# Kernel optimization log

Measured on AMD Instinct MI355X. Metric: run time of the kernel, lower is better.

## Reference

```python
import jax, jax.numpy as jnp
import numpy as np

# ---- static genetic-code tables (stand-in for CODON2ID / ID2AA / SYN_CODON) ----
N_CODONS = 65   # index 0 = pad
N_AA = 24       # ids 0..2 special, 3..22 = 20 amino acids, 23 = stop
_SIZES = np.array([4, 6, 2, 2, 2, 2, 2, 3, 2, 6, 1, 2, 4, 2, 6, 4, 4, 1, 2, 4, 3], dtype=np.int64)  # degeneracy per group (last = stop), sums to 64
_CODON2AA_np = np.concatenate([[0], np.repeat(np.arange(3, 24), _SIZES)])          # [65]
_NSYN_np = np.zeros(N_AA, dtype=np.float32)
_NSYN_np[3:23] = _SIZES[:20]                    # stop (23) and specials (<=2) -> 0, i.e. not in SYN_CODON
CODON2AA = jnp.asarray(_CODON2AA_np)            # [65] int
NSYN_CODON = jnp.asarray(_NSYN_np[_CODON2AA_np])  # [65] f32, n_synonymous for each codon's AA
_starts = 1 + np.concatenate([[0], np.cumsum(_SIZES)[:-1]])
_OFF_AA = np.zeros(N_AA, dtype=np.int64); _OFF_AA[3:24] = _starts
_SZ_AA = np.ones(N_AA, dtype=np.int64);  _SZ_AA[3:24] = _SIZES
OFF_AA = jnp.asarray(_OFF_AA)
SZ_AA = jnp.asarray(_SZ_AA)


def _sequence_rscu(codon_ids, mask):
    """Vectorized compute_sequence_rscu: histogram + per-AA grouped normalization."""
    B = codon_ids.shape[0]
    valid = mask & (codon_ids > 0)
    w = valid.astype(jnp.float32)
    # per-batch codon histogram: scatter-add of 1s over codon ids  [B, 65]
    counts = jnp.zeros((B, N_CODONS), jnp.float32).at[jnp.arange(B)[:, None], codon_ids].add(w)
    # per-AA total count via segment-reduce over the static codon->AA map  [B, 24]
    aa_tot = jnp.zeros((B, N_AA), jnp.float32).at[:, CODON2AA].add(counts)
    tot_c = aa_tot[:, CODON2AA]  # gather AA total back to codon axis  [B, 65]
    # rscu = count * n_synonymous / total_count_of_that_AA (0 where no observations / non-SYN AA)
    rscu = jnp.where(tot_c > 0, counts * NSYN_CODON / jnp.maximum(tot_c, 1.0), 0.0)
    return rscu


def setup_inputs() -> dict:
    key = jax.random.key(0)
    k1, k2, k3, k4, k5 = jax.random.split(key, 5)
    B, L, S = 512, 8192, 5
    target_codon_ids = jax.random.randint(k1, (B, L), 1, N_CODONS)
    aa_ids = CODON2AA[target_codon_ids]                       # consistent AA labels (>=3)
    r = jax.random.randint(k2, (B, L), 0, 6)
    pred_codon_ids = OFF_AA[aa_ids] + r % SZ_AA[aa_ids]       # synonymous predictions (same AA)
    mask = jax.random.uniform(k3, (B, L)) < 0.9
    species_ids = jax.random.randint(k4, (B,), 0, S)
    ref_distributions = jax.random.uniform(k5, (S, N_CODONS), minval=0.0, maxval=2.0)
    return dict(pred_codon_ids=pred_codon_ids, target_codon_ids=target_codon_ids,
                aa_ids=aa_ids, species_ids=species_ids, mask=mask,
                ref_distributions=ref_distributions)


def reference(pred_codon_ids, target_codon_ids, aa_ids, species_ids, mask, ref_distributions):
    pred_rscu = _sequence_rscu(pred_codon_ids, mask)
    target_rscu = _sequence_rscu(target_codon_ids, mask)
    n_species = ref_distributions.shape[0]
    in_range = (species_ids >= 0) & (species_ids < n_species)
    ref_rscu = jnp.where(in_range[:, None],
                         ref_distributions[jnp.clip(species_ids, 0, n_species - 1)], 0.0)
    combined_target = 0.7 * target_rscu + 0.3 * ref_rscu
    p = pred_rscu + 1e-8
    t = combined_target + 1e-8
    p = p / p.sum(axis=1, keepdims=True)
    t = t / t.sum(axis=1, keepdims=True)
    kl_div = (t * jnp.log(t / p)).sum(axis=1)  # [B]
    return kl_div
```

## Files before the change

kernel.cpp:

```cpp
#include <hip/hip_runtime.h>

#define N_CODONS 65
#define N_AA 24

__constant__ int c_codon2aa[N_CODONS] = {
    0,
    3,3,3,3,
    4,4,4,4,4,4,
    5,5,
    6,6,
    7,7,
    8,8,
    9,9,
    10,10,10,
    11,11,
    12,12,12,12,12,12,
    13,
    14,14,
    15,15,15,15,
    16,16,
    17,17,17,17,17,17,
    18,18,18,18,
    19,19,19,19,
    20,
    21,21,
    22,22,22,22,
    23,23,23
};

__constant__ float c_nsyn[N_CODONS] = {
    0.f,
    4.f,4.f,4.f,4.f,
    6.f,6.f,6.f,6.f,6.f,6.f,
    2.f,2.f,
    2.f,2.f,
    2.f,2.f,
    2.f,2.f,
    2.f,2.f,
    3.f,3.f,3.f,
    2.f,2.f,
    6.f,6.f,6.f,6.f,6.f,6.f,
    1.f,
    2.f,2.f,
    4.f,4.f,4.f,4.f,
    2.f,2.f,
    6.f,6.f,6.f,6.f,6.f,6.f,
    4.f,4.f,4.f,4.f,
    4.f,4.f,4.f,4.f,
    1.f,
    2.f,2.f,
    4.f,4.f,4.f,4.f,
    0.f,0.f,0.f
};

__device__ __forceinline__ float wave_sum64(float v) {
#pragma unroll
    for (int off = 32; off > 0; off >>= 1)
        v += __shfl_xor(v, off, 64);
    return v;
}

__global__ __launch_bounds__(1024)
void rscu_kl_kernel(const int* __restrict__ pred,
                    const int* __restrict__ targ,
                    const int* __restrict__ mask,
                    const int* __restrict__ species,
                    const float* __restrict__ ref,
                    float* __restrict__ out,
                    int L, int n_species)
{
    const int b    = blockIdx.x;
    const int tid  = threadIdx.x;
    const int lane = tid & 63;

    __shared__ unsigned int h[2][16][N_CODONS];
    __shared__ float pr[N_CODONS];
    __shared__ float tr[N_CODONS];
    __shared__ float aaP[N_AA], aaT[N_AA];

    for (int i = tid; i < 2 * 16 * N_CODONS; i += 1024)
        ((unsigned int*)h)[i] = 0u;
    if (tid < N_AA) { aaP[tid] = 0.f; aaT[tid] = 0.f; }
    __syncthreads();

    const int4* p4 = (const int4*)(pred + (size_t)b * L);
    const int4* t4 = (const int4*)(targ + (size_t)b * L);
    const int4* m4 = (const int4*)(mask + (size_t)b * L);
    const int nvec = L >> 2;

    unsigned int* hp = &h[0][lane >> 2][0];
    unsigned int* ht = &h[1][lane >> 2][0];
    const unsigned int inc = 1u << ((lane & 3) * 8);

    for (int i = tid; i < nvec; i += 1024) {
        int4 pv = p4[i];
        int4 tv = t4[i];
        int4 mv = m4[i];
        int bp0 = mv.x ? pv.x : 0;  int bt0 = mv.x ? tv.x : 0;
        int bp1 = mv.y ? pv.y : 0;  int bt1 = mv.y ? tv.y : 0;
        int bp2 = mv.z ? pv.z : 0;  int bt2 = mv.z ? tv.z : 0;
        int bp3 = mv.w ? pv.w : 0;  int bt3 = mv.w ? tv.w : 0;
        atomicAdd(hp + bp0, inc);   atomicAdd(ht + bt0, inc);
        atomicAdd(hp + bp1, inc);   atomicAdd(ht + bt1, inc);
        atomicAdd(hp + bp2, inc);   atomicAdd(ht + bt2, inc);
        atomicAdd(hp + bp3, inc);   atomicAdd(ht + bt3, inc);
    }
    __syncthreads();

    if (tid < N_CODONS) {
        unsigned int sp = 0u, st = 0u;
#pragma unroll
        for (int g = 0; g < 16; ++g) {
            unsigned int wp = h[0][g][tid];
            unsigned int wt = h[1][g][tid];
            sp += (wp & 0x00FF00FFu) + ((wp >> 8) & 0x00FF00FFu);
            st += (wt & 0x00FF00FFu) + ((wt >> 8) & 0x00FF00FFu);
        }
        float fcp = (float)((sp & 0xFFFFu) + (sp >> 16));
        float fct = (float)((st & 0xFFFFu) + (st >> 16));
        pr[tid] = fcp;
        tr[tid] = fct;
        int a = c_codon2aa[tid];
        atomicAdd(&aaP[a], fcp);
        atomicAdd(&aaT[a], fct);
    }
    __syncthreads();

    if (tid < N_CODONS) {
        int sp = species[b];
        float rv = (sp >= 0 && sp < n_species) ? ref[sp * N_CODONS + tid] : 0.f;
        int a = c_codon2aa[tid];
        float nsyn = c_nsyn[tid];
        float totP = aaP[a], totT = aaT[a];
        float rscu_p = (totP > 0.f) ? pr[tid] * nsyn / fmaxf(totP, 1.f) : 0.f;
        float rscu_t = (totT > 0.f) ? tr[tid] * nsyn / fmaxf(totT, 1.f) : 0.f;
        pr[tid] = rscu_p + 1e-8f;
        tr[tid] = 0.7f * rscu_t + 0.3f * rv + 1e-8f;
    }
    __syncthreads();

    if (tid < 64) {
        float pv = pr[tid] + (tid == 0 ? pr[64] : 0.f);
        float tv = tr[tid] + (tid == 0 ? tr[64] : 0.f);
        float psum = wave_sum64(pv);
        float tsum = wave_sum64(tv);
        float inv_ps = 1.f / psum;
        float inv_ts = 1.f / tsum;

        float tn = tr[tid] * inv_ts;
        float pn = pr[tid] * inv_ps;
        float kl = tn * __logf(tn / pn);
        if (tid == 0) {
            float tn2 = tr[64] * inv_ts;
            float pn2 = pr[64] * inv_ps;
            kl += tn2 * __logf(tn2 / pn2);
        }
        kl = wave_sum64(kl);
        if (tid == 0) out[b] = kl;
    }
}

extern "C" void kernel_launch(void* const* d_in, const int* in_sizes, int n_in,
                              void* d_out, int out_size, void* d_ws, size_t ws_size,
                              hipStream_t stream) {
    const int* pred    = (const int*)d_in[0];
    const int* targ    = (const int*)d_in[1];
    const int* species = (const int*)d_in[3];
    const int* mask    = (const int*)d_in[4];
    const float* ref   = (const float*)d_in[5];
    float* out         = (float*)d_out;

    const int B = in_sizes[3];
    const int L = in_sizes[0] / B;
    const int n_species = in_sizes[5] / N_CODONS;

    rscu_kl_kernel<<<dim3(B), dim3(1024), 0, stream>>>(
        pred, targ, mask, species, ref, out, L, n_species);
}
```

Baseline: 15.59 us.

## Streamline RSCU epilogue with wave shuffles and wider per-thread loads

The per-AA totals are now computed inside a single wavefront using static offset/size tables and shuffles, replacing shared-memory float atomics and removing one block barrier. The reduction of the two histograms is split across 130 threads, and the species reference value is fetched before the histogram loop so its latency overlaps other work. Each thread now loads two int4 vectors per iteration instead of one, giving more memory-level parallelism. The loop assumes L is divisible by 8.

Result: no change. 15.63 us (+0.2%).

```diff
diff --git a/kernel.cpp b/kernel.cpp
--- a/kernel.cpp
+++ b/kernel.cpp
@@ -53,6 +53,9 @@
     0.f,0.f,0.f
 };
 
+__constant__ int c_off[N_AA] = {0,0,0, 1,5,11,13,15,17,19,21,24,26,32,33,35,39,41,47,51,55,56,58,62};
+__constant__ int c_sz [N_AA] = {1,1,1, 4,6,2,2,2,2,2,3,2,6,1,2,4,2,6,4,4,1,2,4,3};
+
 __device__ __forceinline__ float wave_sum64(float v) {
 #pragma unroll
     for (int off = 32; off > 0; off >>= 1)
@@ -76,87 +79,111 @@
     __shared__ unsigned int h[2][16][N_CODONS];
     __shared__ float pr[N_CODONS];
     __shared__ float tr[N_CODONS];
-    __shared__ float aaP[N_AA], aaT[N_AA];
+
+    float rv = 0.f, rv64 = 0.f;
+    if (tid < 64) {
+        int sp = species[b];
+        if (sp >= 0 && sp < n_species) {
+            rv = ref[sp * N_CODONS + tid];
+            if (tid == 0) rv64 = ref[sp * N_CODONS + 64];
+        }
+    }
 
     for (int i = tid; i < 2 * 16 * N_CODONS; i += 1024)
         ((unsigned int*)h)[i] = 0u;
-    if (tid < N_AA) { aaP[tid] = 0.f; aaT[tid] = 0.f; }
     __syncthreads();
 
-    const int4* p4 = (const int4*)(pred + (size_t)b * L);
-    const int4* t4 = (const int4*)(targ + (size_t)b * L);
-    const int4* m4 = (const int4*)(mask + (size_t)b * L);
-    const int nvec = L >> 2;
+    const size_t rowoff = (size_t)b * L;
+    const int4* p4 = (const int4*)(pred + rowoff);
+    const int4* t4 = (const int4*)(targ + rowoff);
+    const int4* m4 = (const int4*)(mask + rowoff);
 
     unsigned int* hp = &h[0][lane >> 2][0];
     unsigned int* ht = &h[1][lane >> 2][0];
     const unsigned int inc = 1u << ((lane & 3) * 8);
 
-    for (int i = tid; i < nvec; i += 1024) {
-        int4 pv = p4[i];
-        int4 tv = t4[i];
-        int4 mv = m4[i];
-        int bp0 = mv.x ? pv.x : 0;  int bt0 = mv.x ? tv.x : 0;
-        int bp1 = mv.y ? pv.y : 0;  int bt1 = mv.y ? tv.y : 0;
-        int bp2 = mv.z ? pv.z : 0;  int bt2 = mv.z ? tv.z : 0;
-        int bp3 = mv.w ? pv.w : 0;  int bt3 = mv.w ? tv.w : 0;
-        atomicAdd(hp + bp0, inc);   atomicAdd(ht + bt0, inc);
-        atomicAdd(hp + bp1, inc);   atomicAdd(ht + bt1, inc);
-        atomicAdd(hp + bp2, inc);   atomicAdd(ht + bt2, inc);
-        atomicAdd(hp + bp3, inc);   atomicAdd(ht + bt3, inc);
+    for (int e = tid * 8; e < L; e += 8192) {
+        const int v = e >> 2;
+        int4 pv0 = p4[v]; int4 pv1 = p4[v + 1];
+        int4 tv0 = t4[v]; int4 tv1 = t4[v + 1];
+        int4 mv0 = m4[v]; int4 mv1 = m4[v + 1];
+        atomicAdd(hp + (mv0.x ? pv0.x : 0), inc);
+        atomicAdd(ht + (mv0.x ? tv0.x : 0), inc);
+        atomicAdd(hp + (mv0.y ? pv0.y : 0), inc);
+        atomicAdd(ht + (mv0.y ? tv0.y : 0), inc);
+        atomicAdd(hp + (mv0.z ? pv0.z : 0), inc);
+        atomicAdd(ht + (mv0.z ? tv0.z : 0), inc);
+        atomicAdd(hp + (mv0.w ? pv0.w : 0), inc);
+        atomicAdd(ht + (mv0.w ? tv0.w : 0), inc);
+        atomicAdd(hp + (mv1.x ? pv1.x : 0), inc);
+        atomicAdd(ht + (mv1.x ? tv1.x : 0), inc);
+        atomicAdd(hp + (mv1.y ? pv1.y : 0), inc);
+        atomicAdd(ht + (mv1.y ? tv1.y : 0), inc);
+        atomicAdd(hp + (mv1.z ? pv1.z : 0), inc);
+        atomicAdd(ht + (mv1.z ? tv1.z : 0), inc);
+        atomicAdd(hp + (mv1.w ? pv1.w : 0), inc);
+        atomicAdd(ht + (mv1.w ? tv1.w : 0), inc);
     }
     __syncthreads();
 
-    if (tid < N_CODONS) {
-        unsigned int sp = 0u, st = 0u;
+    if (tid < 2 * N_CODONS) {
+        const int which = (tid >= N_CODONS);
+        const int bin   = tid - which * N_CODONS;
+        unsigned int s = 0u;
 #pragma unroll
         for (int g = 0; g < 16; ++g) {
-            unsigned int wp = h[0][g][tid];
-            unsigned int wt = h[1][g][tid];
-            sp += (wp & 0x00FF00FFu) + ((wp >> 8) & 0x00FF00FFu);
-            st += (wt & 0x00FF00FFu) + ((wt >> 8) & 0x00FF00FFu);
-        }
-        float fcp = (float)((sp & 0xFFFFu) + (sp >> 16));
-        float fct = (float)((st & 0xFFFFu) + (st >> 16));
-        pr[tid] = fcp;
-        tr[tid] = fct;
-        int a = c_codon2aa[tid];
-        atomicAdd(&aaP[a], fcp);
-        atomicAdd(&aaT[a], fct);
+            unsigned int w = h[which][g][bin];
+            s += (w & 0x00FF00FFu) + ((w >> 8) & 0x00FF00FFu);
+        }
+        float f = (float)((s & 0xFFFFu) + (s >> 16));
+        if (which) tr[bin] = f; else pr[bin] = f;
     }
     __syncthreads();
 
-    if (tid < N_CODONS) {
-        int sp = species[b];
-        float rv = (sp >= 0 && sp < n_species) ? ref[sp * N_CODONS + tid] : 0.f;
-        int a = c_codon2aa[tid];
-        float nsyn = c_nsyn[tid];
-        float totP = aaP[a], totT = aaT[a];
-        float rscu_p = (totP > 0.f) ? pr[tid] * nsyn / fmaxf(totP, 1.f) : 0.f;
-        float rscu_t = (totT > 0.f) ? tr[tid] * nsyn / fmaxf(totT, 1.f) : 0.f;
-        pr[tid] = rscu_p + 1e-8f;
-        tr[tid] = 0.7f * rscu_t + 0.3f * rv + 1e-8f;
-    }
-    __syncthreads();
-
     if (tid < 64) {
-        float pv = pr[tid] + (tid == 0 ? pr[64] : 0.f);
-        float tv = tr[tid] + (tid == 0 ? tr[64] : 0.f);
-        float psum = wave_sum64(pv);
-        float tsum = wave_sum64(tv);
+        float sumP = 0.f, sumT = 0.f;
+        if (lane < N_AA) {
+            int off = c_off[lane], sz = c_sz[lane];
+            for (int k = 0; k < sz; ++k) {
+                sumP += pr[off + k];
+                sumT += tr[off + k];
+            }
+        }
+        int aa = c_codon2aa[lane];
+        float totP   = __shfl(sumP, aa, 64);
+        float totT   = __shfl(sumT, aa, 64);
+        float totP23 = __shfl(sumP, 23, 64);
+        float totT23 = __shfl(sumT, 23, 64);
+
+        float nsyn = c_nsyn[lane];
+        float rscu_p = (totP > 0.f) ? pr[lane] * nsyn / fmaxf(totP, 1.f) : 0.f;
+        float rscu_t = (totT > 0.f) ? tr[lane] * nsyn / fmaxf(totT, 1.f) : 0.f;
+        float pe = rscu_p + 1e-8f;
+        float te = 0.7f * rscu_t + 0.3f * rv + 1e-8f;
+
+        float pe64 = 0.f, te64 = 0.f;
+        if (lane == 0) {
+            float rp64 = (totP23 > 0.f) ? pr[64] * c_nsyn[64] / fmaxf(totP23, 1.f) : 0.f;
+            float rt64 = (totT23 > 0.f) ? tr[64] * c_nsyn[64] / fmaxf(totT23, 1.f) : 0.f;
+            pe64 = rp64 + 1e-8f;
+            te64 = 0.7f * rt64 + 0.3f * rv64 + 1e-8f;
+        }
+
+        float psum = wave_sum64(pe + pe64);
+        float tsum = wave_sum64(te + te64);
         float inv_ps = 1.f / psum;
         float inv_ts = 1.f / tsum;
 
-        float tn = tr[tid] * inv_ts;
-        float pn = pr[tid] * inv_ps;
+        float tn = te * inv_ts;
+        float pn = pe * inv_ps;
         float kl = tn * __logf(tn / pn);
-        if (tid == 0) {
-            float tn2 = tr[64] * inv_ts;
-            float pn2 = pr[64] * inv_ps;
+        if (lane == 0) {
+            float tn2 = te64 * inv_ts;
+            float pn2 = pe64 * inv_ps;
             kl += tn2 * __logf(tn2 / pn2);
         }
         kl = wave_sum64(kl);
-        if (tid == 0) out[b] = kl;
+        if (lane == 0) out[b] = kl;
     }
 }
 
```
